# Performance work log

Hardware: AMD Instinct MI355X
Metric: run time of the kernel (lower is better)

## Reference

```python
import jax, jax.numpy as jnp
import numpy as np

D_MODEL, N_HEADS, D_K, BASE, EPS = 1024, 16, 64, 10000, 1e-6
SCALE = 1.0 / np.sqrt(D_K)


def rope(x):
    # x: [b, s, h, d]
    b, s, h, d = x.shape
    d2 = d // 2
    theta = 1.0 / (BASE ** (jnp.arange(0, d, 2, dtype=jnp.float32) / d))  # [d2]
    idx_theta = jnp.arange(s, dtype=jnp.float32)[:, None] * theta[None, :]  # [s, d2]
    idx_theta2 = jnp.concatenate([idx_theta, idx_theta], axis=1)  # [s, d]
    cos = jnp.cos(idx_theta2)[None, :, None, :]
    sin = jnp.sin(idx_theta2)[None, :, None, :]
    neg_half = jnp.concatenate([-x[..., d2:], x[..., :d2]], axis=-1)
    return x * cos + neg_half * sin


def setup_inputs() -> dict:
    key = jax.random.key(0)
    ks = jax.random.split(key, 10)
    B, S = 2, 2048
    std = 1.0 / np.sqrt(D_MODEL)
    return {
        "h": jax.random.normal(ks[0], (B, S, D_MODEL), dtype=jnp.float32),
        "wq": jax.random.normal(ks[1], (D_MODEL, N_HEADS * D_K), dtype=jnp.float32) * std,
        "bq": jnp.zeros((N_HEADS * D_K,), dtype=jnp.float32),
        "wk": jax.random.normal(ks[2], (D_MODEL, N_HEADS * D_K), dtype=jnp.float32) * std,
        "bk": jnp.zeros((N_HEADS * D_K,), dtype=jnp.float32),
        "wv": jax.random.normal(ks[3], (D_MODEL, N_HEADS * D_K), dtype=jnp.float32) * std,
        "bv": jnp.zeros((N_HEADS * D_K,), dtype=jnp.float32),
        "wo": jax.random.normal(ks[4], (N_HEADS * D_K, D_MODEL), dtype=jnp.float32) * std,
        "bo": jnp.zeros((D_MODEL,), dtype=jnp.float32),
        "g": jnp.ones((D_MODEL,), dtype=jnp.float32),
    }


def reference(h, wq, bq, wk, bk, wv, bv, wo, bo, g):
    B, S, _ = h.shape
    h_res = h
    # RMSNorm
    hn = h * jax.lax.rsqrt(jnp.mean(h * h, axis=-1, keepdims=True) + EPS) * g
    mh = (B, S, N_HEADS, D_K)
    q = (hn @ wq + bq).reshape(mh)
    k = (hn @ wk + bk).reshape(mh)
    v = (hn @ wv + bv).reshape(mh)
    q, k = rope(q), rope(k)
    attn = jnp.einsum('bihd,bjhd->bhij', q, k) * SCALE
    mask = jnp.tril(jnp.ones((S, S), dtype=bool))
    attn = jnp.where(mask, attn, -jnp.inf)
    attn = jax.nn.softmax(attn, axis=-1)
    out = jnp.einsum('bhij,bjhd->bihd', attn, v).reshape(B, S, N_HEADS * D_K)
    return out @ wo + bo + h_res
```

## Files before the change

kernel.cpp:

```cpp
#include <hip/hip_runtime.h>
#include <hip/hip_bf16.h>

#define D_MODEL 1024
#define NH 16
#define DK 64
#define SEQ 2048
#define BATCH 2
#define NTOK (BATCH * SEQ)
#define EPS 1e-6f

typedef __attribute__((ext_vector_type(4))) float f32x4;
typedef __attribute__((ext_vector_type(16))) float f32x16;
typedef __attribute__((ext_vector_type(8))) short s16x8;
typedef unsigned int u32;
typedef __hip_bfloat16 bf16;

#define AS1 __attribute__((address_space(1)))
#define AS3 __attribute__((address_space(3)))

static __device__ __forceinline__ s16x8 ld8(const bf16* p) {
    return *reinterpret_cast<const s16x8*>(p);
}
static __device__ __forceinline__ float b2f(short s) {
    return __uint_as_float(((u32)(unsigned short)s) << 16);
}

static __device__ __forceinline__ u32 cvtpk(float lo, float hi) {
    u32 r;
    asm volatile("v_cvt_pk_bf16_f32 %0, %1, %2" : "=v"(r) : "v"(lo), "v"(hi));
    return r;
}
static __device__ __forceinline__ void swap32(u32& a, u32& b) {
    asm volatile("v_permlane32_swap_b32 %0, %1" : "+v"(a), "+v"(b));
}
static __device__ __forceinline__ float exp2f_fast(float x) {
    float r;
    asm("v_exp_f32 %0, %1" : "=v"(r) : "v"(x));
    return r;
}
static __device__ __forceinline__ void gld_lds16(const bf16* g, bf16* l) {
    __builtin_amdgcn_global_load_lds((const AS1 void*)g, (AS3 void*)l, 16, 0, 0);
}

union W4 { s16x8 v; u32 w[4]; };

#define LDSW(arr, row, kc) ld8(&arr[(row)][(((kc) ^ ((row) & 7)) << 3)])

__global__ __launch_bounds__(256) void k_prep(const float* __restrict__ h,
                                              const float* __restrict__ g,
                                              const float* __restrict__ wq,
                                              const float* __restrict__ wk,
                                              const float* __restrict__ wv,
                                              const float* __restrict__ wo,
                                              bf16* __restrict__ hn,
                                              bf16* __restrict__ wallT,
                                              float2* __restrict__ tab) {
    const int bid = blockIdx.x;
    const int tid = threadIdx.x;
    if (bid < 4096) {
        const int row = bid;
        const float4 x = reinterpret_cast<const float4*>(h + (size_t)row * D_MODEL)[tid];
        float ss = x.x * x.x + x.y * x.y + x.z * x.z + x.w * x.w;
#pragma unroll
        for (int off = 32; off; off >>= 1) ss += __shfl_xor(ss, off);
        __shared__ float red[4];
        if ((tid & 63) == 0) red[tid >> 6] = ss;
        __syncthreads();
        const float tot = red[0] + red[1] + red[2] + red[3];
        const float rs = rsqrtf(tot * (1.0f / D_MODEL) + EPS);
        const float4 gg = reinterpret_cast<const float4*>(g)[tid];
        bf16* o = hn + (size_t)row * D_MODEL + tid * 4;
        o[0] = __float2bfloat16(x.x * rs * gg.x);
        o[1] = __float2bfloat16(x.y * rs * gg.y);
        o[2] = __float2bfloat16(x.z * rs * gg.z);
        o[3] = __float2bfloat16(x.w * rs * gg.w);
        if (row < 256) {
            const int idx = row * 256 + tid;
            const int s = idx >> 5, i = idx & 31;
            const float theta = __expf(-(float)i * 0.28782313662425572f);
            float sn, cs;
            sincosf((float)s * theta, &sn, &cs);
            tab[idx] = make_float2(cs, sn);
        }
    } else {
        __shared__ float t[32][33];
        const int bid2 = bid - 4096;
        const int kt = (bid2 & 31) * 32;
        const int by = bid2 >> 5;
        const int nt = by * 32;
        const float* W = (by < 32) ? wq : (by < 64) ? wk : (by < 96) ? wv : wo;
        const int nl = nt & (D_MODEL - 1);
        const int tx = tid & 31, ty = tid >> 5;
#pragma unroll
        for (int i = 0; i < 4; i++)
            t[ty + 8 * i][tx] = W[(size_t)(kt + ty + 8 * i) * D_MODEL + nl + tx];
        __syncthreads();
#pragma unroll
        for (int i = 0; i < 4; i++)
            wallT[(size_t)(nt + ty + 8 * i) * D_MODEL + kt + tx] = __float2bfloat16(t[tx][ty + 8 * i]);
    }
}

__global__ __launch_bounds__(256) void k_gemm64_qkv(const bf16* __restrict__ A,
                                                    const bf16* __restrict__ Bt,
                                                    const float* __restrict__ bq,
                                                    const float* __restrict__ bk,
                                                    const float* __restrict__ bv,
                                                    const float2* __restrict__ tab,
                                                    bf16* __restrict__ qb,
                                                    bf16* __restrict__ kpk,
                                                    bf16* __restrict__ vpk) {
    __shared__ __align__(16) char smem[16384];
    bf16(*As)[64] = (bf16(*)[64])smem;
    bf16(*Bs)[64] = (bf16(*)[64])(smem + 8192);
    const int tid = threadIdx.x;
    const int w = tid >> 6, lane = tid & 63, l16 = lane & 15, lq = lane >> 4;
    const int wr = w >> 1, wc = w & 1;
    const int col0 = blockIdx.x * 64;
    const int row0 = blockIdx.y * 64;
    const int grow = lane >> 3;
    const int scol = (((lane & 7) ^ grow) << 3);
    f32x4 acc[2][2];
#pragma unroll
    for (int i = 0; i < 2; i++)
#pragma unroll
        for (int j = 0; j < 2; j++) acc[i][j] = f32x4{0, 0, 0, 0};

    for (int kt = 0; kt < D_MODEL; kt += 64) {
        gld_lds16(A + (size_t)(row0 + w * 16 + grow) * D_MODEL + kt + scol,      &As[w * 16][0]);
        gld_lds16(A + (size_t)(row0 + w * 16 + 8 + grow) * D_MODEL + kt + scol,  &As[w * 16 + 8][0]);
        gld_lds16(Bt + (size_t)(col0 + w * 16 + grow) * D_MODEL + kt + scol,     &Bs[w * 16][0]);
        gld_lds16(Bt + (size_t)(col0 + w * 16 + 8 + grow) * D_MODEL + kt + scol, &Bs[w * 16 + 8][0]);
        __syncthreads();
        s16x8 af[2][2], bfr[2][2];
#pragma unroll
        for (int mi = 0; mi < 2; mi++)
#pragma unroll
            for (int ks = 0; ks < 2; ks++)
                af[mi][ks] = LDSW(As, wr * 32 + mi * 16 + l16, ks * 4 + lq);
#pragma unroll
        for (int ni = 0; ni < 2; ni++)
#pragma unroll
            for (int ks = 0; ks < 2; ks++)
                bfr[ni][ks] = LDSW(Bs, wc * 32 + ni * 16 + l16, ks * 4 + lq);
        __builtin_amdgcn_s_setprio(1);
#pragma unroll
        for (int ks = 0; ks < 2; ks++)
#pragma unroll
            for (int mi = 0; mi < 2; mi++)
#pragma unroll
                for (int ni = 0; ni < 2; ni++)
                    acc[mi][ni] = __builtin_amdgcn_mfma_f32_16x16x32_bf16(af[mi][ks], bfr[ni][ks], acc[mi][ni], 0, 0, 0);
        __builtin_amdgcn_s_setprio(0);
        __syncthreads();
    }

    const int sect = col0 >> 10;
    const int b_ = row0 >> 11;
    const int head = (col0 & 1023) >> 6;
    if (sect == 2) {
        const int e0 = (lq & 1) * 4;
        const int tileL = (row0 & (SEQ - 1)) >> 6;
        bf16* dstH = vpk + ((size_t)(b_ * NH + head) << 17);
#pragma unroll
        for (int ni = 0; ni < 2; ni++) {
            const int dloc = wc * 32 + ni * 16 + l16;
            const float bs = bv[(col0 & 1023) + dloc];
#pragma unroll
            for (int mi = 0; mi < 2; mi++) {
                const int m = wr * 2 + mi;
                size_t off = ((((size_t)(tileL * 2 + (dloc >> 5)) * 4 + m) * 64
                               + ((lq >> 1) & 1) * 32 + (dloc & 31)) << 3) + e0;
                uint2 pv;
                pv.x = cvtpk(acc[mi][ni][0] + bs, acc[mi][ni][1] + bs);
                pv.y = cvtpk(acc[mi][ni][2] + bs, acc[mi][ni][3] + bs);
                *reinterpret_cast<uint2*>(dstH + off) = pv;
            }
        }
        return;
    }
    bf16(*Cs)[72] = (bf16(*)[72])smem;
    const float* bias = (sect == 0) ? bq : bk;
#pragma unroll
    for (int ni = 0; ni < 2; ni++) {
        const int cl = wc * 32 + ni * 16 + l16;
        const float bs = bias[(col0 & 1023) + cl];
#pragma unroll
        for (int mi = 0; mi < 2; mi++) {
            const int rl = wr * 32 + mi * 16 + lq * 4;
#pragma unroll
            for (int r = 0; r < 4; r++)
                Cs[rl + r][cl] = __float2bfloat16(acc[mi][ni][r] + bs);
        }
    }
    __syncthreads();
    const int row = tid >> 2, q = tid & 3;
    const int s_ = (row0 + row) & (SEQ - 1);
    const float2* tb = tab + s_ * 32 + q * 8;
    const float qs = (sect == 0) ? 0.18033688011112042f : 1.0f;
    const s16x8 vlo = ld8(&Cs[row][q * 8]);
    const s16x8 vhi = ld8(&Cs[row][q * 8 + 32]);
    u32 plo[4], phi[4];
#pragma unroll
    for (int e2 = 0; e2 < 4; e2++) {
        float a[2], b[2];
#pragma unroll
        for (int k = 0; k < 2; k++) {
            const int e = e2 * 2 + k;
            const float2 cs = tb[e];
            const float x1 = b2f(vlo[e]), x2 = b2f(vhi[e]);
            a[k] = (x1 * cs.x - x2 * cs.y) * qs;
            b[k] = (x2 * cs.x + x1 * cs.y) * qs;
        }
        plo[e2] = cvtpk(a[0], a[1]);
        phi[e2] = cvtpk(b[0], b[1]);
    }
    if (sect == 0) {
        bf16* qdst = qb + (((size_t)(b_ * NH + head) * SEQ + s_) << 6);
        *reinterpret_cast<uint4*>(qdst + q * 8)      = make_uint4(plo[0], plo[1], plo[2], plo[3]);
        *reinterpret_cast<uint4*>(qdst + 32 + q * 8) = make_uint4(phi[0], phi[1], phi[2], phi[3]);
    } else {
        bf16* kdst = kpk + ((size_t)(b_ * NH + head) << 17);
        const int jb = s_ >> 5, j31 = s_ & 31;
        const size_t offL = (((size_t)(jb * 4 + (q >> 1)) * 64 + (q & 1) * 32 + j31) << 3);
        const size_t offH = (((size_t)(jb * 4 + ((q + 4) >> 1)) * 64 + ((q + 4) & 1) * 32 + j31) << 3);
        *reinterpret_cast<uint4*>(kdst + offL) = make_uint4(plo[0], plo[1], plo[2], plo[3]);
        *reinterpret_cast<uint4*>(kdst + offH) = make_uint4(phi[0], phi[1], phi[2], phi[3]);
    }
}

__global__ __launch_bounds__(256) void k_attn7(const bf16* __restrict__ qg,
                                               const bf16* __restrict__ kp,
                                               const bf16* __restrict__ vp,
                                               bf16* __restrict__ ao) {
    __shared__ float part[2][64][35];
    const int tid = threadIdx.x;
    const int wid = tid >> 6;
    const int lane = tid & 63;
    const int l31 = lane & 31;
    const int hi = lane >> 5;
    const int pi = wid >> 1;
    const int h = wid & 1;
    const int bid = blockIdx.x;
    const int pb  = (bid >> 3) & 31;
    const int bh  = (bid & 7) + ((bid >> 8) << 3);
    const int pos = 2 * pb + pi;
    const int qw = pos << 5;
    const int qrow = qw + l31;

    const bf16* qptr = qg + (((size_t)bh * SEQ + qrow) << 6) + 8 * hi;
    s16x8 qf[4];
#pragma unroll
    for (int t = 0; t < 4; t++) qf[t] = ld8(qptr + 16 * t);

    f32x16 o0, o1;
#pragma unroll
    for (int r = 0; r < 16; r++) { o0[r] = 0.0f; o1[r] = 0.0f; }
    float m_run = -1e30f, l_run = 0.0f;

    const int nfull = qw >> 6;
    const int ntot  = (qw + 95) >> 6;
    const bf16* kbase = kp + ((size_t)bh << 17);
    const bf16* vbase = vp + ((size_t)bh << 17);

    s16x8 kA[8], kB[8], vC[8];

    auto att_step = [&](s16x8(&KC)[8], s16x8(&KN)[8], const int kt) {
        const int kb = kt << 6;
#pragma unroll
        for (int t = 0; t < 8; t++)
            vC[t] = ld8(vbase + (((size_t)(kt * 8 + t) * 64 + lane) << 3));
        f32x16 s0, s1;
#pragma unroll
        for (int r = 0; r < 16; r++) { s0[r] = 0.0f; s1[r] = 0.0f; }
        __builtin_amdgcn_s_setprio(1);
#pragma unroll
        for (int t = 0; t < 4; t++) {
            s0 = __builtin_amdgcn_mfma_f32_32x32x16_bf16(KC[t],     qf[t], s0, 0, 0, 0);
            s1 = __builtin_amdgcn_mfma_f32_32x32x16_bf16(KC[4 + t], qf[t], s1, 0, 0, 0);
        }
        __builtin_amdgcn_s_setprio(0);
        const int ktn = (kt + 2 < ntot) ? kt + 2 : kt;
#pragma unroll
        for (int t = 0; t < 8; t++)
            KN[t] = ld8(kbase + (((size_t)(ktn * 8 + t) * 64 + lane) << 3));
        float p[32];
#pragma unroll
        for (int r = 0; r < 16; r++) { p[r] = s0[r]; p[16 + r] = s1[r]; }
        if (kt >= nfull) {
#pragma unroll
            for (int r = 0; r < 32; r++) {
                const int j = kb + 8 * (r >> 2) + (r & 3) + 4 * hi;
                if (j > qrow) p[r] = -3.0e38f;
            }
        }
        float m16[16];
#pragma unroll
        for (int r = 0; r < 16; r++) m16[r] = fmaxf(p[r], p[r + 16]);
#pragma unroll
        for (int r = 0; r < 8; r++) m16[r] = fmaxf(m16[r], m16[r + 8]);
#pragma unroll
        for (int r = 0; r < 4; r++) m16[r] = fmaxf(m16[r], m16[r + 4]);
        float mx = fmaxf(fmaxf(m16[0], m16[1]), fmaxf(m16[2], m16[3]));
        mx = fmaxf(mx, __shfl_xor(mx, 32));
        if (!__all(mx <= m_run + 8.0f)) {
            const float mn = fmaxf(m_run, mx);
            const float alpha = exp2f_fast(m_run - mn);
            m_run = mn;
            l_run *= alpha;
#pragma unroll
            for (int r = 0; r < 16; r++) { o0[r] *= alpha; o1[r] *= alpha; }
        }
        float s4[4] = {0, 0, 0, 0};
#pragma unroll
        for (int r = 0; r < 32; r++) { p[r] = exp2f_fast(p[r] - m_run); s4[r & 3] += p[r]; }
        float rs = (s4[0] + s4[1]) + (s4[2] + s4[3]);
        rs += __shfl_xor(rs, 32);
        l_run += rs;
        u32 pk_[16];
#pragma unroll
        for (int a = 0; a < 8; a++) {
            pk_[2 * a]     = cvtpk(p[4 * a],     p[4 * a + 1]);
            pk_[2 * a + 1] = cvtpk(p[4 * a + 2], p[4 * a + 3]);
        }
        __builtin_amdgcn_s_setprio(1);
#pragma unroll
        for (int m = 0; m < 4; m++) {
            u32 b0 = pk_[4 * m],     b2 = pk_[4 * m + 2];
            u32 b1 = pk_[4 * m + 1], b3 = pk_[4 * m + 3];
            swap32(b0, b2);
            swap32(b1, b3);
            W4 B; B.w[0] = b0; B.w[1] = b1; B.w[2] = b2; B.w[3] = b3;
            o0 = __builtin_amdgcn_mfma_f32_32x32x16_bf16(vC[m],     B.v, o0, 0, 0, 0);
            o1 = __builtin_amdgcn_mfma_f32_32x32x16_bf16(vC[4 + m], B.v, o1, 0, 0, 0);
        }
        __builtin_amdgcn_s_setprio(0);
    };

    int kt = h;
    if (kt < ntot) {
#pragma unroll
        for (int t = 0; t < 8; t++) kA[t] = ld8(kbase + (((size_t)(kt * 8 + t) * 64 + lane) << 3));
        for (;;) {
            att_step(kA, kB, kt); kt += 2; if (kt >= ntot) break;
            att_step(kB, kA, kt); kt += 2; if (kt >= ntot) break;
        }
    }

    if (h == 0) {
        float* dst = &part[pi][lane][0];
#pragma unroll
        for (int r4 = 0; r4 < 4; r4++) {
            *reinterpret_cast<float4*>(dst + r4 * 4) =
                make_float4(o0[4 * r4], o0[4 * r4 + 1], o0[4 * r4 + 2], o0[4 * r4 + 3]);
            *reinterpret_cast<float4*>(dst + 16 + r4 * 4) =
                make_float4(o1[4 * r4], o1[4 * r4 + 1], o1[4 * r4 + 2], o1[4 * r4 + 3]);
        }
        dst[32] = m_run;
        dst[33] = l_run;
    }
    __syncthreads();
    if (h == 0) return;

    const float* src = &part[pi][lane][0];
    const float mA = src[32], lA = src[33];
    const float mN = fmaxf(mA, m_run);
    const float aA = exp2f_fast(mA - mN);
    const float aB = exp2f_fast(m_run - mN);
    const float inv = 1.0f / (lA * aA + l_run * aB);

    const int b_ = bh >> 4, h_ = bh & (NH - 1);
    bf16* orow = ao + (((size_t)(b_ * SEQ + qrow)) << 10) + (h_ << 6);
#pragma unroll
    for (int g = 0; g < 4; g++) {
        {
            uint2 val;
            val.x = cvtpk((src[4 * g] * aA + o0[4 * g] * aB) * inv,
                          (src[4 * g + 1] * aA + o0[4 * g + 1] * aB) * inv);
            val.y = cvtpk((src[4 * g + 2] * aA + o0[4 * g + 2] * aB) * inv,
                          (src[4 * g + 3] * aA + o0[4 * g + 3] * aB) * inv);
            *reinterpret_cast<uint2*>(orow + 8 * g + 4 * hi) = val;
        }
        {
            uint2 val;
            val.x = cvtpk((src[16 + 4 * g] * aA + o1[4 * g] * aB) * inv,
                          (src[16 + 4 * g + 1] * aA + o1[4 * g + 1] * aB) * inv);
            val.y = cvtpk((src[16 + 4 * g + 2] * aA + o1[4 * g + 2] * aB) * inv,
                          (src[16 + 4 * g + 3] * aA + o1[4 * g + 3] * aB) * inv);
            *reinterpret_cast<uint2*>(orow + 32 + 8 * g + 4 * hi) = val;
        }
    }
}

__global__ __launch_bounds__(256) void k_gemm64_out(const bf16* __restrict__ A,
                                                    const bf16* __restrict__ Bt,
                                                    const float* __restrict__ bo,
                                                    const float* __restrict__ hres,
                                                    float* __restrict__ out) {
    __shared__ __align__(16) char smem[16384];
    bf16(*As)[64] = (bf16(*)[64])smem;
    bf16(*Bs)[64] = (bf16(*)[64])(smem + 8192);
    const int tid = threadIdx.x;
    const int w = tid >> 6, lane = tid & 63, l16 = lane & 15, lq = lane >> 4;
    const int wr = w >> 1, wc = w & 1;
    const int col0 = blockIdx.x * 64;
    const int row0 = blockIdx.y * 64;
    const int grow = lane >> 3;
    const int scol = (((lane & 7) ^ grow) << 3);
    f32x4 acc[2][2];
#pragma unroll
    for (int i = 0; i < 2; i++)
#pragma unroll
        for (int j = 0; j < 2; j++) acc[i][j] = f32x4{0, 0, 0, 0};

    for (int kt = 0; kt < D_MODEL; kt += 64) {
        gld_lds16(A + (size_t)(row0 + w * 16 + grow) * D_MODEL + kt + scol,      &As[w * 16][0]);
        gld_lds16(A + (size_t)(row0 + w * 16 + 8 + grow) * D_MODEL + kt + scol,  &As[w * 16 + 8][0]);
        gld_lds16(Bt + (size_t)(col0 + w * 16 + grow) * D_MODEL + kt + scol,     &Bs[w * 16][0]);
        gld_lds16(Bt + (size_t)(col0 + w * 16 + 8 + grow) * D_MODEL + kt + scol, &Bs[w * 16 + 8][0]);
        __syncthreads();
        s16x8 af[2][2], bfr[2][2];
#pragma unroll
        for (int mi = 0; mi < 2; mi++)
#pragma unroll
            for (int ks = 0; ks < 2; ks++)
                af[mi][ks] = LDSW(As, wr * 32 + mi * 16 + l16, ks * 4 + lq);
#pragma unroll
        for (int ni = 0; ni < 2; ni++)
#pragma unroll
            for (int ks = 0; ks < 2; ks++)
                bfr[ni][ks] = LDSW(Bs, wc * 32 + ni * 16 + l16, ks * 4 + lq);
        __builtin_amdgcn_s_setprio(1);
#pragma unroll
        for (int ks = 0; ks < 2; ks++)
#pragma unroll
            for (int mi = 0; mi < 2; mi++)
#pragma unroll
                for (int ni = 0; ni < 2; ni++)
                    acc[mi][ni] = __builtin_amdgcn_mfma_f32_16x16x32_bf16(af[mi][ks], bfr[ni][ks], acc[mi][ni], 0, 0, 0);
        __builtin_amdgcn_s_setprio(0);
        __syncthreads();
    }
#pragma unroll
    for (int ni = 0; ni < 2; ni++) {
        const int col = col0 + wc * 32 + ni * 16 + l16;
        const float bs = bo[col];
#pragma unroll
        for (int mi = 0; mi < 2; mi++) {
#pragma unroll
            for (int r = 0; r < 4; r++) {
                const int row = row0 + wr * 32 + mi * 16 + lq * 4 + r;
                out[(size_t)row * D_MODEL + col] =
                    acc[mi][ni][r] + bs + hres[(size_t)row * D_MODEL + col];
            }
        }
    }
}

extern "C" void kernel_launch(void* const* d_in, const int* in_sizes, int n_in,
                              void* d_out, int out_size, void* d_ws, size_t ws_size,
                              hipStream_t stream) {
    (void)in_sizes; (void)n_in; (void)out_size; (void)ws_size;
    const float* h  = (const float*)d_in[0];
    const float* wq = (const float*)d_in[1];
    const float* bq = (const float*)d_in[2];
    const float* wk = (const float*)d_in[3];
    const float* bk = (const float*)d_in[4];
    const float* wv = (const float*)d_in[5];
    const float* bv = (const float*)d_in[6];
    const float* wo = (const float*)d_in[7];
    const float* bo = (const float*)d_in[8];
    const float* g  = (const float*)d_in[9];
    float* out = (float*)d_out;

    char* ws = (char*)d_ws;
    size_t off = 0;
    auto carve = [&](size_t bytes) {
        void* p = ws + off;
        off += (bytes + 255) & ~(size_t)255;
        return p;
    };
    bf16* hn    = (bf16*)carve((size_t)NTOK * D_MODEL * 2);
    bf16* wallT = (bf16*)carve((size_t)4 * D_MODEL * D_MODEL * 2);
    bf16* wqkvT = wallT;
    bf16* woT   = wallT + (size_t)3 * D_MODEL * D_MODEL;
    bf16* qb    = (bf16*)carve((size_t)BATCH * NH * SEQ * DK * 2);
    bf16* kpk   = (bf16*)carve((size_t)BATCH * NH * SEQ * DK * 2);
    bf16* vpk   = (bf16*)carve((size_t)BATCH * NH * SEQ * DK * 2);
    bf16* ao    = (bf16*)carve((size_t)NTOK * D_MODEL * 2);
    float2* tab = (float2*)carve((size_t)SEQ * 32 * sizeof(float2));

    k_prep<<<8192, 256, 0, stream>>>(h, g, wq, wk, wv, wo, hn, wallT, tab);
    k_gemm64_qkv<<<dim3(48, 64), 256, 0, stream>>>(hn, wqkvT, bq, bk, bv, tab, qb, kpk, vpk);
    k_attn7<<<1024, 256, 0, stream>>>(qb, kpk, vpk, ao);
    k_gemm64_out<<<dim3(16, 64), 256, 0, stream>>>(ao, woT, bo, h, out);
}
```

Measured before the change: 120.1 us.

## Share double-buffered K/V tiles in LDS across four query warps

Rewrites the attention kernel so that each block handles 128 query rows with four warps, one per 32-row slice. Instead of splitting the key range between warp pairs and merging partial softmax state through shared memory, all four warps now read the same K/V tile from LDS. That tile is loaded with direct global-to-LDS copies and double-buffered against compute. Blocks are issued in reverse query order to balance the causal triangle, and the final cross-warp merge is gone. The trade-offs are half as many blocks, a barrier on every key tile, and extra fully masked tiles for the lower warps in each block.

```diff
diff --git a/kernel.cpp b/kernel.cpp
--- a/kernel.cpp
+++ b/kernel.cpp
@@ -229,23 +229,20 @@
     }
 }
 
-__global__ __launch_bounds__(256) void k_attn7(const bf16* __restrict__ qg,
+__global__ __launch_bounds__(256) void k_attn8(const bf16* __restrict__ qg,
                                                const bf16* __restrict__ kp,
                                                const bf16* __restrict__ vp,
                                                bf16* __restrict__ ao) {
-    __shared__ float part[2][64][35];
+    __shared__ __align__(16) bf16 kv[2][2][4096];
     const int tid = threadIdx.x;
-    const int wid = tid >> 6;
+    const int w = tid >> 6;
     const int lane = tid & 63;
     const int l31 = lane & 31;
     const int hi = lane >> 5;
-    const int pi = wid >> 1;
-    const int h = wid & 1;
     const int bid = blockIdx.x;
-    const int pb  = (bid >> 3) & 31;
-    const int bh  = (bid & 7) + ((bid >> 8) << 3);
-    const int pos = 2 * pb + pi;
-    const int qw = pos << 5;
+    const int qb  = 15 - ((bid >> 3) & 15);
+    const int bh  = (bid & 7) + ((bid >> 7) << 3);
+    const int qw = qb * 128 + w * 32;
     const int qrow = qw + l31;
 
     const bf16* qptr = qg + (((size_t)bh * SEQ + qrow) << 6) + 8 * hi;
@@ -259,17 +256,27 @@
     float m_run = -1e30f, l_run = 0.0f;
 
     const int nfull = qw >> 6;
-    const int ntot  = (qw + 95) >> 6;
+    const int ntot  = 2 * qb + 2;
     const bf16* kbase = kp + ((size_t)bh << 17);
     const bf16* vbase = vp + ((size_t)bh << 17);
 
-    s16x8 kA[8], kB[8], vC[8];
-
-    auto att_step = [&](s16x8(&KC)[8], s16x8(&KN)[8], const int kt) {
-        const int kb = kt << 6;
-#pragma unroll
-        for (int t = 0; t < 8; t++)
-            vC[t] = ld8(vbase + (((size_t)(kt * 8 + t) * 64 + lane) << 3));
+    auto STAGE = [&](int buf, int kt) {
+        gld_lds16(kbase + (((size_t)(kt * 8 + w)) * 64 + lane) * 8,     &kv[buf][0][w * 512]);
+        gld_lds16(kbase + (((size_t)(kt * 8 + w + 4)) * 64 + lane) * 8, &kv[buf][0][(w + 4) * 512]);
+        gld_lds16(vbase + (((size_t)(kt * 8 + w)) * 64 + lane) * 8,     &kv[buf][1][w * 512]);
+        gld_lds16(vbase + (((size_t)(kt * 8 + w + 4)) * 64 + lane) * 8, &kv[buf][1][(w + 4) * 512]);
+    };
+
+    STAGE(0, 0);
+    __syncthreads();
+    int buf = 0;
+    for (int kt = 0; kt < ntot; kt++) {
+        if (kt + 1 < ntot) STAGE(buf ^ 1, kt + 1);
+        s16x8 KC[8], VC[8];
+#pragma unroll
+        for (int t = 0; t < 8; t++) KC[t] = ld8(&kv[buf][0][(t * 64 + lane) * 8]);
+#pragma unroll
+        for (int t = 0; t < 8; t++) VC[t] = ld8(&kv[buf][1][(t * 64 + lane) * 8]);
         f32x16 s0, s1;
 #pragma unroll
         for (int r = 0; r < 16; r++) { s0[r] = 0.0f; s1[r] = 0.0f; }
@@ -280,10 +287,7 @@
             s1 = __builtin_amdgcn_mfma_f32_32x32x16_bf16(KC[4 + t], qf[t], s1, 0, 0, 0);
         }
         __builtin_amdgcn_s_setprio(0);
-        const int ktn = (kt + 2 < ntot) ? kt + 2 : kt;
-#pragma unroll
-        for (int t = 0; t < 8; t++)
-            KN[t] = ld8(kbase + (((size_t)(ktn * 8 + t) * 64 + lane) << 3));
+        const int kb = kt << 6;
         float p[32];
 #pragma unroll
         for (int r = 0; r < 16; r++) { p[r] = s0[r]; p[16 + r] = s1[r]; }
@@ -331,62 +335,29 @@
             swap32(b0, b2);
             swap32(b1, b3);
             W4 B; B.w[0] = b0; B.w[1] = b1; B.w[2] = b2; B.w[3] = b3;
-            o0 = __builtin_amdgcn_mfma_f32_32x32x16_bf16(vC[m],     B.v, o0, 0, 0, 0);
-            o1 = __builtin_amdgcn_mfma_f32_32x32x16_bf16(vC[4 + m], B.v, o1, 0, 0, 0);
+            o0 = __builtin_amdgcn_mfma_f32_32x32x16_bf16(VC[m],     B.v, o0, 0, 0, 0);
+            o1 = __builtin_amdgcn_mfma_f32_32x32x16_bf16(VC[4 + m], B.v, o1, 0, 0, 0);
         }
         __builtin_amdgcn_s_setprio(0);
-    };
-
-    int kt = h;
-    if (kt < ntot) {
-#pragma unroll
-        for (int t = 0; t < 8; t++) kA[t] = ld8(kbase + (((size_t)(kt * 8 + t) * 64 + lane) << 3));
-        for (;;) {
-            att_step(kA, kB, kt); kt += 2; if (kt >= ntot) break;
-            att_step(kB, kA, kt); kt += 2; if (kt >= ntot) break;
-        }
-    }
-
-    if (h == 0) {
-        float* dst = &part[pi][lane][0];
-#pragma unroll
-        for (int r4 = 0; r4 < 4; r4++) {
-            *reinterpret_cast<float4*>(dst + r4 * 4) =
-                make_float4(o0[4 * r4], o0[4 * r4 + 1], o0[4 * r4 + 2], o0[4 * r4 + 3]);
-            *reinterpret_cast<float4*>(dst + 16 + r4 * 4) =
-                make_float4(o1[4 * r4], o1[4 * r4 + 1], o1[4 * r4 + 2], o1[4 * r4 + 3]);
-        }
-        dst[32] = m_run;
-        dst[33] = l_run;
-    }
-    __syncthreads();
-    if (h == 0) return;
-
-    const float* src = &part[pi][lane][0];
-    const float mA = src[32], lA = src[33];
-    const float mN = fmaxf(mA, m_run);
-    const float aA = exp2f_fast(mA - mN);
-    const float aB = exp2f_fast(m_run - mN);
-    const float inv = 1.0f / (lA * aA + l_run * aB);
-
+        __syncthreads();
+        buf ^= 1;
+    }
+
+    const float inv = 1.0f / l_run;
     const int b_ = bh >> 4, h_ = bh & (NH - 1);
     bf16* orow = ao + (((size_t)(b_ * SEQ + qrow)) << 10) + (h_ << 6);
 #pragma unroll
     for (int g = 0; g < 4; g++) {
         {
             uint2 val;
-            val.x = cvtpk((src[4 * g] * aA + o0[4 * g] * aB) * inv,
-                          (src[4 * g + 1] * aA + o0[4 * g + 1] * aB) * inv);
-            val.y = cvtpk((src[4 * g + 2] * aA + o0[4 * g + 2] * aB) * inv,
-                          (src[4 * g + 3] * aA + o0[4 * g + 3] * aB) * inv);
+            val.x = cvtpk(o0[4 * g] * inv, o0[4 * g + 1] * inv);
+            val.y = cvtpk(o0[4 * g + 2] * inv, o0[4 * g + 3] * inv);
             *reinterpret_cast<uint2*>(orow + 8 * g + 4 * hi) = val;
         }
         {
             uint2 val;
-            val.x = cvtpk((src[16 + 4 * g] * aA + o1[4 * g] * aB) * inv,
-                          (src[16 + 4 * g + 1] * aA + o1[4 * g + 1] * aB) * inv);
-            val.y = cvtpk((src[16 + 4 * g + 2] * aA + o1[4 * g + 2] * aB) * inv,
-                          (src[16 + 4 * g + 3] * aA + o1[4 * g + 3] * aB) * inv);
+            val.x = cvtpk(o1[4 * g] * inv, o1[4 * g + 1] * inv);
+            val.y = cvtpk(o1[4 * g + 2] * inv, o1[4 * g + 3] * inv);
             *reinterpret_cast<uint2*>(orow + 32 + 8 * g + 4 * hi) = val;
         }
     }
@@ -492,6 +463,6 @@
 
     k_prep<<<8192, 256, 0, stream>>>(h, g, wq, wk, wv, wo, hn, wallT, tab);
     k_gemm64_qkv<<<dim3(48, 64), 256, 0, stream>>>(hn, wqkvT, bq, bk, bv, tab, qb, kpk, vpk);
-    k_attn7<<<1024, 256, 0, stream>>>(qb, kpk, vpk, ao);
+    k_attn8<<<512, 256, 0, stream>>>(qb, kpk, vpk, ao);
     k_gemm64_out<<<dim3(16, 64), 256, 0, stream>>>(ao, woT, bo, h, out);
 }
```

Result: slower. 126.1 us (+4.9%).
